# Optimization experiments

Measured on AMD Instinct MI355X. Metric: run time of the kernel, lower is better.

Reference implementation:

```python
import jax, jax.numpy as jnp
import numpy as np

SHAPES = np.array([[92, 92], [46, 46], [23, 23], [12, 12]], dtype=np.int32)
EMB, HID, H, L, P = 256, 256, 8, 4, 4


def setup_inputs() -> dict:
    key = jax.random.key(0)
    ks = jax.random.split(key, 10)
    I = int(SHAPES.prod(-1).sum())  # 11253 total pyramid pixels
    B, N = 2, I                      # dense encoder-style queries
    img = jax.random.normal(ks[0], (B, I, EMB), jnp.float32)
    queries = jax.random.normal(ks[1], (B, N, EMB), jnp.float32)
    reference_points = jax.random.uniform(ks[2], (B, N, 2), jnp.float32)
    s = 0.02  # keep offsets small so sampling points stay near [0,1]
    W_img = s * jax.random.normal(ks[3], (EMB, HID), jnp.float32)
    b_img = s * jax.random.normal(ks[4], (HID,), jnp.float32)
    W_q = s * jax.random.normal(ks[5], (EMB, H * L * P * 3), jnp.float32)
    b_q = s * jax.random.normal(ks[6], (H * L * P * 3,), jnp.float32)
    W_out = s * jax.random.normal(ks[7], (HID, EMB), jnp.float32)
    b_out = s * jax.random.normal(ks[8], (EMB,), jnp.float32)
    return dict(img=img, shapes=jnp.asarray(SHAPES), queries=queries,
                reference_points=reference_points, W_img=W_img, b_img=b_img,
                W_q=W_q, b_q=b_q, W_out=W_out, b_out=b_out)


def _msda(img_p, shapes_np, sp, aw):
    # img_p: [B,I,H,Cp], sp: [B,N,H,L,P,2] in [0,1] (x,y), aw: [B,N,H,L,P]
    B, I, Hh, Cp = img_p.shape
    N = sp.shape[1]
    imgT = img_p.transpose(0, 2, 1, 3)       # [B,H,I,Cp]
    awT = aw.transpose(0, 2, 1, 3, 4)        # [B,H,N,L,P]
    out = jnp.zeros((B, Hh, N, Cp), img_p.dtype)
    start = 0
    for l in range(shapes_np.shape[0]):
        h, w = int(shapes_np[l, 0]), int(shapes_np[l, 1])
        lvl = imgT[:, :, start:start + h * w]            # [B,H,h*w,Cp]
        start += h * w
        pts = sp[:, :, :, l].transpose(0, 2, 1, 3, 4)    # [B,H,N,P,2]
        # grid_sample(align_corners=True, border): pix = p*(size-1), clamped
        x = jnp.clip(pts[..., 0] * (w - 1), 0.0, w - 1)
        y = jnp.clip(pts[..., 1] * (h - 1), 0.0, h - 1)
        x0 = jnp.floor(x); y0 = jnp.floor(y)
        wx = x - x0; wy = y - y0
        x0i = x0.astype(jnp.int32); y0i = y0.astype(jnp.int32)
        x1i = jnp.minimum(x0i + 1, w - 1); y1i = jnp.minimum(y0i + 1, h - 1)

        def gat(yi, xi):
            idx = (yi * w + xi).reshape(B, Hh, N * P)
            g = jnp.take_along_axis(lvl, idx[..., None], axis=2)
            return g.reshape(B, Hh, N, P, Cp)

        v = (gat(y0i, x0i) * ((1 - wy) * (1 - wx))[..., None]
             + gat(y0i, x1i) * ((1 - wy) * wx)[..., None]
             + gat(y1i, x0i) * (wy * (1 - wx))[..., None]
             + gat(y1i, x1i) * (wy * wx)[..., None])     # [B,H,N,P,Cp]
        out = out + jnp.einsum('bhnpc,bhnp->bhnc', v, awT[:, :, :, l])
    return out.transpose(0, 2, 1, 3)                      # [B,N,H,Cp]


def reference(img, shapes, queries, reference_points, W_img, b_img, W_q, b_q, W_out, b_out):
    shapes_np = np.asarray(jax.device_get(shapes))
    B, I, C = img.shape
    N = queries.shape[1]
    Cp = HID // H
    img_p = (img @ W_img + b_img).reshape(B, I, H, Cp)
    qp = (queries @ W_q + b_q).reshape(B, N, H, L, P, 3)
    offsets = qp[..., :2]
    aw = jax.nn.softmax(qp[..., 2].reshape(B, N, H, L * P), axis=-1).reshape(B, N, H, L, P)
    sp = reference_points[:, :, None, None, None, :] + offsets  # [B,N,H,L,P,2]
    out = _msda(img_p, shapes_np, sp, aw)                        # [B,N,H,Cp]
    return out.reshape(B, N, HID) @ W_out + b_out
```

## Files before the change

### kernel.cpp

```cpp
#include <hip/hip_runtime.h>
#include <math.h>

#define NB    2
#define NQ    11253
#define NEMB  256
#define NHID  256
#define NH    8
#define NCP   32
#define MROWS (NB * NQ)
#define NGRP  (NB * NQ * NH)

__device__ __constant__ int LVL_H[4]     = {92, 46, 23, 12};
__device__ __constant__ int LVL_W[4]     = {92, 46, 23, 12};
__device__ __constant__ int LVL_START[4] = {0, 8464, 10580, 11109};

typedef float  f32x4   __attribute__((ext_vector_type(4)));
typedef __bf16 bf16x8  __attribute__((ext_vector_type(8)));
typedef __bf16 bf16x4v __attribute__((ext_vector_type(4)));
typedef short  s16x8   __attribute__((ext_vector_type(8)));

__global__ __launch_bounds__(256) void convert_w_T(
    const float* __restrict__ W_img, const float* __restrict__ W_q,
    const float* __restrict__ W_out,
    __bf16* __restrict__ WiTh, __bf16* __restrict__ WiTl,
    __bf16* __restrict__ WqTh, __bf16* __restrict__ WqTl,
    __bf16* __restrict__ WoTh, __bf16* __restrict__ WoTl)
{
    int idx = blockIdx.x * 256 + threadIdx.x;
    const float* W; __bf16 *Th, *Tl; int Nn, r;
    if (idx < 8192)       { W = W_img; Th = WiTh; Tl = WiTl; Nn = 256; r = idx; }
    else if (idx < 20480) { W = W_q;   Th = WqTh; Tl = WqTl; Nn = 384; r = idx - 8192; }
    else                  { W = W_out; Th = WoTh; Tl = WoTl; Nn = 256; r = idx - 20480; }
    const int n  = r % Nn;
    const int k0 = (r / Nn) * 8;
    bf16x8 h, l;
    #pragma unroll
    for (int j = 0; j < 8; ++j) {
        float v = W[(size_t)(k0 + j) * Nn + n];
        __bf16 hh = (__bf16)v;
        h[j] = hh; l[j] = (__bf16)(v - (float)hh);
    }
    *(bf16x8*)(Th + (size_t)n * 256 + k0) = h;
    *(bf16x8*)(Tl + (size_t)n * 256 + k0) = l;
}

#define BM 64
#define BN 64
#define BK 32
#define LDK 40

template<bool PREA>
__global__ __launch_bounds__(256) void gemm64(
    const float* __restrict__ A32,
    const __bf16* __restrict__ AhG, const __bf16* __restrict__ AlG,
    const __bf16* __restrict__ BhT, const __bf16* __restrict__ BlT,
    const float* __restrict__ bias, float* __restrict__ C,
    int M, int N, int K)
{
    __shared__ __bf16 Ah[BM * LDK];
    __shared__ __bf16 Al[BM * LDK];
    __shared__ __bf16 Bh[BN * LDK];
    __shared__ __bf16 Bl[BN * LDK];

    const int t    = threadIdx.x;
    const int brow = blockIdx.x * BM;
    const int bcol = blockIdx.y * BN;
    const int wave = t >> 6;
    const int lane = t & 63;
    const int wr   = (wave >> 1) * 32;
    const int wc   = (wave & 1) * 32;
    const int l15  = lane & 15;
    const int l4   = lane >> 4;

    f32x4 acc[2][2] = {};

    const int sr = t >> 2;
    const int sk = (t & 3) * 8;
    const int grow = brow + sr;

    for (int k0 = 0; k0 < K; k0 += BK) {
        if constexpr (PREA) {
            s16x8 h = {}, l = {};
            if (grow < M) {
                h = *(const s16x8*)(AhG + (size_t)grow * K + k0 + sk);
                l = *(const s16x8*)(AlG + (size_t)grow * K + k0 + sk);
            }
            *(s16x8*)&Ah[sr * LDK + sk] = h;
            *(s16x8*)&Al[sr * LDK + sk] = l;
        } else {
            float va[8];
            if (grow < M) {
                const float* ap = A32 + (size_t)grow * K + k0 + sk;
                *(float4*)&va[0] = *(const float4*)(ap + 0);
                *(float4*)&va[4] = *(const float4*)(ap + 4);
            } else {
                #pragma unroll
                for (int i = 0; i < 8; ++i) va[i] = 0.f;
            }
            bf16x8 h, l;
            #pragma unroll
            for (int i = 0; i < 8; ++i) {
                __bf16 hh = (__bf16)va[i];
                h[i] = hh; l[i] = (__bf16)(va[i] - (float)hh);
            }
            *(bf16x8*)&Ah[sr * LDK + sk] = h;
            *(bf16x8*)&Al[sr * LDK + sk] = l;
        }
        {
            *(s16x8*)&Bh[sr * LDK + sk] =
                *(const s16x8*)(BhT + (size_t)(bcol + sr) * K + k0 + sk);
            *(s16x8*)&Bl[sr * LDK + sk] =
                *(const s16x8*)(BlT + (size_t)(bcol + sr) * K + k0 + sk);
        }
        __syncthreads();

        s16x8 a_h[2], a_l[2], b_h[2], b_l[2];
        #pragma unroll
        for (int mi = 0; mi < 2; ++mi) {
            int off = (wr + mi * 16 + l15) * LDK + l4 * 8;
            a_h[mi] = *(s16x8*)&Ah[off];
            a_l[mi] = *(s16x8*)&Al[off];
        }
        #pragma unroll
        for (int ni = 0; ni < 2; ++ni) {
            int off = (wc + ni * 16 + l15) * LDK + l4 * 8;
            b_h[ni] = *(s16x8*)&Bh[off];
            b_l[ni] = *(s16x8*)&Bl[off];
        }
        #pragma unroll
        for (int mi = 0; mi < 2; ++mi)
            #pragma unroll
            for (int ni = 0; ni < 2; ++ni) {
                acc[mi][ni] = __builtin_amdgcn_mfma_f32_16x16x32_bf16(a_h[mi], b_h[ni], acc[mi][ni], 0, 0, 0);
                acc[mi][ni] = __builtin_amdgcn_mfma_f32_16x16x32_bf16(a_h[mi], b_l[ni], acc[mi][ni], 0, 0, 0);
                acc[mi][ni] = __builtin_amdgcn_mfma_f32_16x16x32_bf16(a_l[mi], b_h[ni], acc[mi][ni], 0, 0, 0);
            }
        __syncthreads();
    }

    #pragma unroll
    for (int ni = 0; ni < 2; ++ni) {
        const int col = bcol + wc + ni * 16 + l15;
        const float bv = bias[col];
        #pragma unroll
        for (int mi = 0; mi < 2; ++mi) {
            #pragma unroll
            for (int j = 0; j < 4; ++j) {
                int row = brow + wr + mi * 16 + l4 * 4 + j;
                if (row < M) C[(size_t)row * N + col] = acc[mi][ni][j] + bv;
            }
        }
    }
}

__global__ __launch_bounds__(256) void msda_kernel(
    const float* __restrict__ img_p, const float* __restrict__ qp,
    const float* __restrict__ refp,
    __bf16* __restrict__ outH, __bf16* __restrict__ outL)
{
    __shared__ int smem[16][32][8];
    const int t  = threadIdx.x;
    const int t3 = t & 7;
    const int g  = t >> 3;
    int gid = blockIdx.x * 32 + g;
    const bool valid = gid < NGRP;
    if (!valid) gid = NGRP - 1;
    const int h  = gid & 7;
    const int bn = gid >> 3;
    const int b  = (bn >= NQ) ? 1 : 0;

    const float* q  = qp + (size_t)bn * 384 + h * 48;
    const float rx = refp[bn * 2 + 0];
    const float ry = refp[bn * 2 + 1];

    const float ox0 = q[t3 * 3 + 0],        oy0 = q[t3 * 3 + 1],        sc0 = q[t3 * 3 + 2];
    const float ox1 = q[(t3 + 8) * 3 + 0],  oy1 = q[(t3 + 8) * 3 + 1],  sc1 = q[(t3 + 8) * 3 + 2];

    float mx = fmaxf(sc0, sc1);
    mx = fmaxf(mx, __shfl_xor(mx, 1, 8));
    mx = fmaxf(mx, __shfl_xor(mx, 2, 8));
    mx = fmaxf(mx, __shfl_xor(mx, 4, 8));
    const float e0 = __expf(sc0 - mx);
    const float e1 = __expf(sc1 - mx);
    float sum = e0 + e1;
    sum += __shfl_xor(sum, 1, 8);
    sum += __shfl_xor(sum, 2, 8);
    sum += __shfl_xor(sum, 4, 8);
    const float inv = 1.0f / sum;

    #pragma unroll
    for (int which = 0; which < 2; ++which) {
        const int   s  = which ? (t3 + 8) : t3;
        const float ox = which ? ox1 : ox0;
        const float oy = which ? oy1 : oy0;
        const float aw = (which ? e1 : e0) * inv;
        const int l  = s >> 2;
        const int hh = LVL_H[l], ww = LVL_W[l], st = LVL_START[l];
        float x = (rx + ox) * (float)(ww - 1);
        float y = (ry + oy) * (float)(hh - 1);
        x = fminf(fmaxf(x, 0.f), (float)(ww - 1));
        y = fminf(fmaxf(y, 0.f), (float)(hh - 1));
        const float x0f = floorf(x), y0f = floorf(y);
        const int   x0 = (int)x0f,  y0 = (int)y0f;
        const float wx = x - x0f,   wy = y - y0f;
        const int dxb = (x0 < ww - 1) ? (NH * NCP * 4) : 0;
        const int dyb = (y0 < hh - 1) ? (ww * NH * NCP * 4) : 0;
        const int o00 = (st + y0 * ww + x0) * (NH * NCP * 4);
        const float u0 = aw * (1.f - wx), u1 = aw * wx;
        int4 pa = make_int4(o00, dxb, dyb, __float_as_int(u0 * (1.f - wy)));
        int4 pb = make_int4(__float_as_int(u1 * (1.f - wy)),
                            __float_as_int(u0 * wy),
                            __float_as_int(u1 * wy), 0);
        *(int4*)&smem[s][g][0] = pa;
        *(int4*)&smem[s][g][4] = pb;
    }
    __syncthreads();

    const char* base = (const char*)img_p
        + (((size_t)b * NQ * (NH * NCP) + h * NCP + t3 * 4) * 4);
    f32x4 acc = {0.f, 0.f, 0.f, 0.f};
    #pragma unroll
    for (int s = 0; s < 16; ++s) {
        const int4 pa = *(int4*)&smem[s][g][0];
        const int4 pb = *(int4*)&smem[s][g][4];
        const int o00 = pa.x;
        const int o01 = o00 + pa.y;
        const int o10 = o00 + pa.z;
        const int o11 = o10 + pa.y;
        const f32x4 v00 = *(const f32x4*)(base + o00);
        const f32x4 v01 = *(const f32x4*)(base + o01);
        const f32x4 v10 = *(const f32x4*)(base + o10);
        const f32x4 v11 = *(const f32x4*)(base + o11);
        acc += v00 * __int_as_float(pa.w);
        acc += v01 * __int_as_float(pb.x);
        acc += v10 * __int_as_float(pb.y);
        acc += v11 * __int_as_float(pb.z);
    }
    if (valid) {
        bf16x4v hv, lv;
        #pragma unroll
        for (int j = 0; j < 4; ++j) {
            __bf16 hh = (__bf16)acc[j];
            hv[j] = hh; lv[j] = (__bf16)(acc[j] - (float)hh);
        }
        const size_t o = (size_t)bn * NHID + h * NCP + t3 * 4;
        *(bf16x4v*)(outH + o) = hv;
        *(bf16x4v*)(outL + o) = lv;
    }
}

extern "C" void kernel_launch(void* const* d_in, const int* in_sizes, int n_in,
                              void* d_out, int out_size, void* d_ws, size_t ws_size,
                              hipStream_t stream) {
    const float* img     = (const float*)d_in[0];
    const float* queries = (const float*)d_in[2];
    const float* refp    = (const float*)d_in[3];
    const float* W_img   = (const float*)d_in[4];
    const float* b_img   = (const float*)d_in[5];
    const float* W_q     = (const float*)d_in[6];
    const float* b_q     = (const float*)d_in[7];
    const float* W_out   = (const float*)d_in[8];
    const float* b_out   = (const float*)d_in[9];
    float* out = (float*)d_out;

    const size_t NA = (size_t)MROWS * 256;
    float*  img_p = (float*)d_ws;
    float*  qp    = img_p + NA;
    __bf16* msdaH = (__bf16*)(qp + (size_t)MROWS * 384);
    __bf16* msdaL = msdaH + NA;
    __bf16* WiTh  = msdaL + NA;
    __bf16* WiTl  = WiTh + 256 * 256;
    __bf16* WqTh  = WiTl + 256 * 256;
    __bf16* WqTl  = WqTh + 384 * 256;
    __bf16* WoTh  = WqTl + 384 * 256;
    __bf16* WoTl  = WoTh + 256 * 256;

    const int gRows = (MROWS + BM - 1) / BM;

    convert_w_T<<<112, 256, 0, stream>>>(W_img, W_q, W_out,
                                         WiTh, WiTl, WqTh, WqTl, WoTh, WoTl);
    gemm64<false><<<dim3(gRows, 4), 256, 0, stream>>>(
        img, nullptr, nullptr, WiTh, WiTl, b_img, img_p, MROWS, 256, 256);
    gemm64<false><<<dim3(gRows, 6), 256, 0, stream>>>(
        queries, nullptr, nullptr, WqTh, WqTl, b_q, qp, MROWS, 384, 256);
    msda_kernel<<<(NGRP + 31) / 32, 256, 0, stream>>>(img_p, qp, refp, msdaH, msdaL);
    gemm64<true><<<dim3(gRows, 4), 256, 0, stream>>>(
        nullptr, msdaH, msdaL, WoTh, WoTl, b_out, out, MROWS, 256, 256);
}
```

Measured before the change: 229.9 us.

## Widen GEMM tiles to cover full output width and pre-pack weights per K-chunk

The three projection GEMMs now compute a 64-row by full-N (256, or 192 for the q projection) tile per block, instead of 64x64 tiles. This means each A row block is read and split into hi/lo bf16 only once or twice rather than four to six times. Weights are repacked into K-chunk-major layout so one thread loads a contiguous 32-element column slice. The trade-off is more accumulators per wave, larger LDS use, and fewer blocks, which may lower occupancy.

```diff
diff --git a/kernel.cpp b/kernel.cpp
--- a/kernel.cpp
+++ b/kernel.cpp
@@ -40,57 +40,55 @@
         __bf16 hh = (__bf16)v;
         h[j] = hh; l[j] = (__bf16)(v - (float)hh);
     }
-    *(bf16x8*)(Th + (size_t)n * 256 + k0) = h;
-    *(bf16x8*)(Tl + (size_t)n * 256 + k0) = l;
-}
-
-#define BM 64
-#define BN 64
-#define BK 32
+    const size_t dst = ((size_t)(k0 >> 5) * Nn + n) * 32 + (k0 & 31);
+    *(bf16x8*)(Th + dst) = h;
+    *(bf16x8*)(Tl + dst) = l;
+}
+
 #define LDK 40
 
-template<bool PREA>
-__global__ __launch_bounds__(256) void gemm64(
+template<int NCOLS, bool PREA>
+__global__ __launch_bounds__(256) void gemm_fullN(
     const float* __restrict__ A32,
     const __bf16* __restrict__ AhG, const __bf16* __restrict__ AlG,
-    const __bf16* __restrict__ BhT, const __bf16* __restrict__ BlT,
+    const __bf16* __restrict__ BhP, const __bf16* __restrict__ BlP,
     const float* __restrict__ bias, float* __restrict__ C,
-    int M, int N, int K)
+    int M, int NTOT)
 {
-    __shared__ __bf16 Ah[BM * LDK];
-    __shared__ __bf16 Al[BM * LDK];
-    __shared__ __bf16 Bh[BN * LDK];
-    __shared__ __bf16 Bl[BN * LDK];
-
-    const int t    = threadIdx.x;
-    const int brow = blockIdx.x * BM;
-    const int bcol = blockIdx.y * BN;
-    const int wave = t >> 6;
-    const int lane = t & 63;
-    const int wr   = (wave >> 1) * 32;
-    const int wc   = (wave & 1) * 32;
-    const int l15  = lane & 15;
-    const int l4   = lane >> 4;
-
-    f32x4 acc[2][2] = {};
-
-    const int sr = t >> 2;
-    const int sk = (t & 3) * 8;
+    constexpr int NCW = NCOLS / 4;
+    constexpr int NC  = NCW / 16;
+    __shared__ __bf16 Ah[64 * LDK];
+    __shared__ __bf16 Al[64 * LDK];
+    __shared__ __bf16 Bh[NCOLS * LDK];
+    __shared__ __bf16 Bl[NCOLS * LDK];
+
+    const int t      = threadIdx.x;
+    const int brow   = blockIdx.x * 64;
+    const int colOff = blockIdx.y * NCOLS;
+    const int wave   = t >> 6;
+    const int lane   = t & 63;
+    const int l15    = lane & 15;
+    const int l4     = lane >> 4;
+
+    f32x4 acc[4][NC] = {};
+
+    const int sr   = t >> 2;
+    const int sk   = (t & 3) * 8;
     const int grow = brow + sr;
 
-    for (int k0 = 0; k0 < K; k0 += BK) {
+    for (int k0 = 0; k0 < 256; k0 += 32) {
         if constexpr (PREA) {
             s16x8 h = {}, l = {};
             if (grow < M) {
-                h = *(const s16x8*)(AhG + (size_t)grow * K + k0 + sk);
-                l = *(const s16x8*)(AlG + (size_t)grow * K + k0 + sk);
+                h = *(const s16x8*)(AhG + (size_t)grow * 256 + k0 + sk);
+                l = *(const s16x8*)(AlG + (size_t)grow * 256 + k0 + sk);
             }
             *(s16x8*)&Ah[sr * LDK + sk] = h;
             *(s16x8*)&Al[sr * LDK + sk] = l;
         } else {
             float va[8];
             if (grow < M) {
-                const float* ap = A32 + (size_t)grow * K + k0 + sk;
+                const float* ap = A32 + (size_t)grow * 256 + k0 + sk;
                 *(float4*)&va[0] = *(const float4*)(ap + 0);
                 *(float4*)&va[4] = *(const float4*)(ap + 4);
             } else {
@@ -106,48 +104,55 @@
             *(bf16x8*)&Ah[sr * LDK + sk] = h;
             *(bf16x8*)&Al[sr * LDK + sk] = l;
         }
-        {
-            *(s16x8*)&Bh[sr * LDK + sk] =
-                *(const s16x8*)(BhT + (size_t)(bcol + sr) * K + k0 + sk);
-            *(s16x8*)&Bl[sr * LDK + sk] =
-                *(const s16x8*)(BlT + (size_t)(bcol + sr) * K + k0 + sk);
+        if (t < NCOLS) {
+            const size_t pb = ((size_t)(k0 >> 5) * NTOT + colOff + t) * 32;
+            const __bf16* hp = BhP + pb;
+            const __bf16* lp = BlP + pb;
+            s16x8 h0 = *(const s16x8*)(hp +  0), h1 = *(const s16x8*)(hp +  8);
+            s16x8 h2 = *(const s16x8*)(hp + 16), h3 = *(const s16x8*)(hp + 24);
+            s16x8 l0 = *(const s16x8*)(lp +  0), l1 = *(const s16x8*)(lp +  8);
+            s16x8 l2 = *(const s16x8*)(lp + 16), l3 = *(const s16x8*)(lp + 24);
+            __bf16* dh = &Bh[t * LDK];
+            *(s16x8*)(dh +  0) = h0;  *(s16x8*)(dh +  8) = h1;
+            *(s16x8*)(dh + 16) = h2;  *(s16x8*)(dh + 24) = h3;
+            __bf16* dl = &Bl[t * LDK];
+            *(s16x8*)(dl +  0) = l0;  *(s16x8*)(dl +  8) = l1;
+            *(s16x8*)(dl + 16) = l2;  *(s16x8*)(dl + 24) = l3;
         }
         __syncthreads();
 
-        s16x8 a_h[2], a_l[2], b_h[2], b_l[2];
-        #pragma unroll
-        for (int mi = 0; mi < 2; ++mi) {
-            int off = (wr + mi * 16 + l15) * LDK + l4 * 8;
+        s16x8 a_h[4], a_l[4];
+        #pragma unroll
+        for (int mi = 0; mi < 4; ++mi) {
+            int off = (mi * 16 + l15) * LDK + l4 * 8;
             a_h[mi] = *(s16x8*)&Ah[off];
             a_l[mi] = *(s16x8*)&Al[off];
         }
         #pragma unroll
-        for (int ni = 0; ni < 2; ++ni) {
-            int off = (wc + ni * 16 + l15) * LDK + l4 * 8;
-            b_h[ni] = *(s16x8*)&Bh[off];
-            b_l[ni] = *(s16x8*)&Bl[off];
-        }
-        #pragma unroll
-        for (int mi = 0; mi < 2; ++mi)
+        for (int ni = 0; ni < NC; ++ni) {
+            int off = (wave * NCW + ni * 16 + l15) * LDK + l4 * 8;
+            s16x8 b_h = *(s16x8*)&Bh[off];
+            s16x8 b_l = *(s16x8*)&Bl[off];
             #pragma unroll
-            for (int ni = 0; ni < 2; ++ni) {
-                acc[mi][ni] = __builtin_amdgcn_mfma_f32_16x16x32_bf16(a_h[mi], b_h[ni], acc[mi][ni], 0, 0, 0);
-                acc[mi][ni] = __builtin_amdgcn_mfma_f32_16x16x32_bf16(a_h[mi], b_l[ni], acc[mi][ni], 0, 0, 0);
-                acc[mi][ni] = __builtin_amdgcn_mfma_f32_16x16x32_bf16(a_l[mi], b_h[ni], acc[mi][ni], 0, 0, 0);
-            }
+            for (int mi = 0; mi < 4; ++mi) {
+                acc[mi][ni] = __builtin_amdgcn_mfma_f32_16x16x32_bf16(a_h[mi], b_h, acc[mi][ni], 0, 0, 0);
+                acc[mi][ni] = __builtin_amdgcn_mfma_f32_16x16x32_bf16(a_h[mi], b_l, acc[mi][ni], 0, 0, 0);
+                acc[mi][ni] = __builtin_amdgcn_mfma_f32_16x16x32_bf16(a_l[mi], b_h, acc[mi][ni], 0, 0, 0);
+            }
+        }
         __syncthreads();
     }
 
     #pragma unroll
-    for (int ni = 0; ni < 2; ++ni) {
-        const int col = bcol + wc + ni * 16 + l15;
-        const float bv = bias[col];
-        #pragma unroll
-        for (int mi = 0; mi < 2; ++mi) {
+    for (int ni = 0; ni < NC; ++ni) {
+        const int gcol = colOff + wave * NCW + ni * 16 + l15;
+        const float bv = bias[gcol];
+        #pragma unroll
+        for (int mi = 0; mi < 4; ++mi) {
             #pragma unroll
             for (int j = 0; j < 4; ++j) {
-                int row = brow + wr + mi * 16 + l4 * 4 + j;
-                if (row < M) C[(size_t)row * N + col] = acc[mi][ni][j] + bv;
+                int row = brow + mi * 16 + l4 * 4 + j;
+                if (row < M) C[(size_t)row * NTOT + gcol] = acc[mi][ni][j] + bv;
             }
         }
     }
@@ -275,15 +280,15 @@
     __bf16* WoTh  = WqTl + 384 * 256;
     __bf16* WoTl  = WoTh + 256 * 256;
 
-    const int gRows = (MROWS + BM - 1) / BM;
+    const int gRows = (MROWS + 63) / 64;
 
     convert_w_T<<<112, 256, 0, stream>>>(W_img, W_q, W_out,
                                          WiTh, WiTl, WqTh, WqTl, WoTh, WoTl);
-    gemm64<false><<<dim3(gRows, 4), 256, 0, stream>>>(
-        img, nullptr, nullptr, WiTh, WiTl, b_img, img_p, MROWS, 256, 256);
-    gemm64<false><<<dim3(gRows, 6), 256, 0, stream>>>(
-        queries, nullptr, nullptr, WqTh, WqTl, b_q, qp, MROWS, 384, 256);
+    gemm_fullN<256, false><<<dim3(gRows, 1), 256, 0, stream>>>(
+        img, nullptr, nullptr, WiTh, WiTl, b_img, img_p, MROWS, 256);
+    gemm_fullN<192, false><<<dim3(gRows, 2), 256, 0, stream>>>(
+        queries, nullptr, nullptr, WqTh, WqTl, b_q, qp, MROWS, 384);
     msda_kernel<<<(NGRP + 31) / 32, 256, 0, stream>>>(img_p, qp, refp, msdaH, msdaL);
-    gemm64<true><<<dim3(gRows, 4), 256, 0, stream>>>(
-        nullptr, msdaH, msdaL, WoTh, WoTl, b_out, out, MROWS, 256, 256);
-}
+    gemm_fullN<256, true><<<dim3(gRows, 1), 256, 0, stream>>>(
+        nullptr, msdaH, msdaL, WoTh, WoTl, b_out, out, MROWS, 256);
+}
```

After: 234.4 us. No clear change (+1.9%).
